# Kernel tuning notes

Hardware: AMD Instinct MI355X
Metric: run time of the kernel (lower is better)

## Reference

```python
import jax, jax.numpy as jnp
import numpy as np
import math

DIM = 384
HEADS = 12
WIN = (12, 12)
N = WIN[0] * WIN[1]  # 144
TABLE = (2 * WIN[0] - 1) * (2 * WIN[1] - 1)  # 529
B_ = 512
NW = 16
CPB_HIDDEN = 512


def setup_inputs() -> dict:
    key = jax.random.key(0)
    ks = jax.random.split(key, 12)
    x = jax.random.normal(ks[0], (B_, N, DIM), dtype=jnp.float32)
    relative_coords_table = jax.random.uniform(ks[1], (1, 2 * WIN[0] - 1, 2 * WIN[1] - 1, 2), dtype=jnp.float32) * 2.0 - 1.0
    relative_position_index = jax.random.randint(ks[2], (N, N), 0, TABLE, dtype=jnp.int64)
    mask = jnp.zeros((NW, N, N), dtype=jnp.float32)
    # learned params
    qkv_w = jax.random.normal(ks[3], (3 * DIM, DIM), dtype=jnp.float32) * (1.0 / math.sqrt(DIM))
    q_bias = jnp.zeros((DIM,), dtype=jnp.float32)
    k_bias = jnp.zeros((DIM,), dtype=jnp.float32)
    v_bias = jnp.zeros((DIM,), dtype=jnp.float32)
    logit_scale = jnp.full((HEADS, 1, 1), math.log(10.0), dtype=jnp.float32)
    cpb_w1 = jax.random.normal(ks[4], (CPB_HIDDEN, 2), dtype=jnp.float32) * 0.5
    cpb_b1 = jnp.zeros((CPB_HIDDEN,), dtype=jnp.float32)
    cpb_w2 = jax.random.normal(ks[5], (HEADS, CPB_HIDDEN), dtype=jnp.float32) * (1.0 / math.sqrt(CPB_HIDDEN))
    proj_w = jax.random.normal(ks[6], (DIM, DIM), dtype=jnp.float32) * (1.0 / math.sqrt(DIM))
    proj_b = jnp.zeros((DIM,), dtype=jnp.float32)
    return {
        'x': x,
        'relative_coords_table': relative_coords_table,
        'relative_position_index': relative_position_index,
        'mask': mask,
        'qkv_w': qkv_w, 'q_bias': q_bias, 'k_bias': k_bias, 'v_bias': v_bias,
        'logit_scale': logit_scale,
        'cpb_w1': cpb_w1, 'cpb_b1': cpb_b1, 'cpb_w2': cpb_w2,
        'proj_w': proj_w, 'proj_b': proj_b,
    }


def reference(x, relative_coords_table, relative_position_index, mask,
              qkv_w, q_bias, k_bias, v_bias, logit_scale,
              cpb_w1, cpb_b1, cpb_w2, proj_w, proj_b):
    Bw, n, C = x.shape
    H = HEADS
    d = C // H
    qkv_bias = jnp.concatenate([q_bias, k_bias, v_bias])
    qkv = x @ qkv_w.T + qkv_bias  # (Bw, n, 3C)
    qkv = qkv.reshape(Bw, n, 3, H, d).transpose(2, 0, 3, 1, 4)  # (3, Bw, H, n, d)
    q, k, v = qkv[0], qkv[1], qkv[2]
    # cosine attention
    qn = q / jnp.linalg.norm(q, axis=-1, keepdims=True)
    kn = k / jnp.linalg.norm(k, axis=-1, keepdims=True)
    attn = jnp.einsum('bhnd,bhmd->bhnm', qn, kn)
    scale = jnp.exp(jnp.minimum(logit_scale, math.log(1.0 / 0.01)))  # (H,1,1)
    attn = attn * scale[None]
    # CPB-MLP relative position bias
    h1 = jax.nn.relu(relative_coords_table @ cpb_w1.T + cpb_b1)  # (1,23,23,512)
    table = (h1 @ cpb_w2.T).reshape(-1, H)  # (529, H)
    rpb = table[relative_position_index.reshape(-1)].reshape(n, n, H)
    rpb = 16.0 * jax.nn.sigmoid(rpb.transpose(2, 0, 1))  # (H, n, n)
    attn = attn + rpb[None]
    # shifted-window mask
    nW = mask.shape[0]
    attn = attn.reshape(Bw // nW, nW, H, n, n) + mask[None, :, None]
    attn = attn.reshape(Bw, H, n, n)
    attn = jax.nn.softmax(attn, axis=-1)
    out = jnp.einsum('bhnm,bhmd->bhnd', attn, v)
    out = out.transpose(0, 2, 1, 3).reshape(Bw, n, C)
    out = out @ proj_w.T + proj_b
    return out
```

## Files before the change

### kernel.cpp

```cpp
#include <hip/hip_runtime.h>

#define DIMC 384
#define NHEADS 12
#define NTOK 144
#define TABLEN 529
#define BWIN 512
#define NWIN 16
#define CPBH 512

typedef unsigned short u16;
typedef unsigned int u32;
typedef __attribute__((ext_vector_type(8))) short short8;
typedef __attribute__((ext_vector_type(4))) float f32x4;

#define MFMA(a, b, c) __builtin_amdgcn_mfma_f32_16x16x32_bf16((a), (b), (c), 0, 0, 0)

__device__ __forceinline__ u16 f2bf(float f) {
  union { float f; u32 u; } v; v.f = f;
  u32 r = v.u + 0x7fffu + ((v.u >> 16) & 1u);
  return (u16)(r >> 16);
}
__device__ __forceinline__ u32 pk2(float a, float b) {
  return (u32)f2bf(a) | ((u32)f2bf(b) << 16);
}
__device__ __forceinline__ u32 cvtpk(float lo, float hi) {
  u32 r;
  asm("v_cvt_pk_bf16_f32 %0, %1, %2" : "=v"(r) : "v"(lo), "v"(hi));
  return r;
}

__global__ __launch_bounds__(256) void cvt_bf16(const float* __restrict__ in,
                                                u16* __restrict__ out, int n8) {
  int i = blockIdx.x * 256 + threadIdx.x;
  if (i >= n8) return;
  const float4* p = (const float4*)(in + (size_t)i * 8);
  float4 a = p[0], b = p[1];
  uint4 r;
  r.x = pk2(a.x, a.y); r.y = pk2(a.z, a.w);
  r.z = pk2(b.x, b.y); r.w = pk2(b.z, b.w);
  *(uint4*)(out + (size_t)i * 8) = r;
}

__global__ __launch_bounds__(256) void cpb_kernel(const float* __restrict__ rct,
                                                  const float* __restrict__ w1,
                                                  const float* __restrict__ b1,
                                                  const float* __restrict__ w2,
                                                  const float* __restrict__ logit_scale,
                                                  float* __restrict__ bias_tab,
                                                  float* __restrict__ scalev) {
  __shared__ float h1[CPBH];
  int i = blockIdx.x;
  int tid = threadIdx.x;
  if (i == 0 && tid < NHEADS)
    scalev[tid] = __expf(fminf(logit_scale[tid], 4.60517018598809f));
  float c0 = rct[2 * i], c1 = rct[2 * i + 1];
  for (int k = tid; k < CPBH; k += 256)
    h1[k] = fmaxf(0.f, fmaf(c0, w1[2 * k], fmaf(c1, w1[2 * k + 1], b1[k])));
  __syncthreads();
  int wv = tid >> 6, lane = tid & 63;
#pragma unroll
  for (int hh = 0; hh < 3; ++hh) {
    int h = wv * 3 + hh;
    const float* w2h = w2 + (size_t)h * CPBH;
    float acc = 0.f;
#pragma unroll
    for (int k = 0; k < CPBH; k += 64) acc = fmaf(h1[k + lane], w2h[k + lane], acc);
    acc += __shfl_xor(acc, 1); acc += __shfl_xor(acc, 2); acc += __shfl_xor(acc, 4);
    acc += __shfl_xor(acc, 8); acc += __shfl_xor(acc, 16); acc += __shfl_xor(acc, 32);
    if (lane == 0) bias_tab[i * NHEADS + h] = 16.f / (1.f + __expf(-acc));
  }
}

__global__ __launch_bounds__(256) void cbias_kernel(const int* __restrict__ rpi,
                                                    const float* __restrict__ bias_tab,
                                                    const float* __restrict__ mask,
                                                    float* __restrict__ cb) {
  int e4 = blockIdx.x * 256 + threadIdx.x;
  if (e4 >= NWIN * NHEADS * NTOK * NTOK / 4) return;
  int m0 = (e4 * 4) % NTOK;
  int t = (e4 * 4) / NTOK;
  int n = t % NTOK; t /= NTOK;
  int h = t % NHEADS;
  int w = t / NHEADS;
  int4 idx = *(const int4*)(rpi + n * NTOK + m0);
  float4 mk = *(const float4*)(mask + ((size_t)(w * NTOK + n)) * NTOK + m0);
  float4 r;
  r.x = bias_tab[idx.x * NHEADS + h] + mk.x;
  r.y = bias_tab[idx.y * NHEADS + h] + mk.y;
  r.z = bias_tab[idx.z * NHEADS + h] + mk.z;
  r.w = bias_tab[idx.w * NHEADS + h] + mk.w;
  *(float4*)(cb + (size_t)e4 * 4) = r;
}

__global__ __launch_bounds__(576) void attn_fused(
    const u16* __restrict__ xb, const u16* __restrict__ wb,
    const float* __restrict__ q_bias, const float* __restrict__ k_bias,
    const float* __restrict__ v_bias, const float* __restrict__ cb,
    const float* __restrict__ scalev, u16* __restrict__ ctx) {
  __shared__ u16 smem[22656];
  u16* qn = smem;
  u16* kn = smem + 5760;
  u16* vT = smem + 11520;
  u16* Pc = smem + 16896;
  u16* xs = smem;
  u16* wsm = smem + 9216;

  int bid = blockIdx.x;
  int xcd = bid & 7;
  int i = bid >> 3;
  int wsub = i / 192;
  int j = i - wsub * 192;
  int bI = j / 6;
  int hp = j - bI * 6;
  int w = xcd * 2 + wsub;
  int b = bI * NWIN + w;
  int h0 = hp * 2;

  int tid = threadIdx.x;
  int lane = tid & 63, wv = tid >> 6;
  int g = lane >> 4, c = lane & 15;
  int rbase = wv * 16;
  int wr3 = wv / 3, wc3 = wv % 3;

  f32x4 acc[3][4];
#pragma unroll
  for (int mi = 0; mi < 3; ++mi)
#pragma unroll
    for (int ni = 0; ni < 4; ++ni) acc[mi][ni] = (f32x4){0.f, 0.f, 0.f, 0.f};

  int r4 = tid >> 2, b4 = tid & 3;
  bool hasW1 = tid < 192;
  int wr1 = 144 + r4;
  int wg0 = (r4 >> 6) * DIMC + (h0 + ((r4 >> 5) & 1)) * 32 + (r4 & 31);
  int wg1 = (wr1 >> 6) * DIMC + (h0 + ((wr1 >> 5) & 1)) * 32 + (wr1 & 31);
  const u16* xg = xb + ((size_t)b * NTOK + r4) * DIMC + b4 * 8;
  const u16* wgp0 = wb + (size_t)wg0 * DIMC + b4 * 8;
  const u16* wgp1 = wb + (size_t)wg1 * DIMC + b4 * 8;
  int xo0 = r4 * 64 + 8 * (b4 ^ (r4 & 7));
  int xo1 = r4 * 64 + 8 * ((b4 + 4) ^ (r4 & 7));
  int w1o0 = wr1 * 64 + 8 * (b4 ^ (wr1 & 7));
  int w1o1 = wr1 * 64 + 8 * ((b4 + 4) ^ (wr1 & 7));

  uint4 pxA, pw0A, pw1A, pxB, pw0B, pw1B;
  pxA = *(const uint4*)(xg);
  pw0A = *(const uint4*)(wgp0);
  if (hasW1) pw1A = *(const uint4*)(wgp1);
  pxB = *(const uint4*)(xg + 32);
  pw0B = *(const uint4*)(wgp0 + 32);
  if (hasW1) pw1B = *(const uint4*)(wgp1 + 32);

#pragma unroll
  for (int tt = 0; tt < 6; ++tt) {
    *(uint4*)(xs + xo0) = pxA;
    *(uint4*)(wsm + xo0) = pw0A;
    if (hasW1) *(uint4*)(wsm + w1o0) = pw1A;
    __syncthreads();
    if (tt < 5) {
      int k0 = (2 * tt + 2) * 32;
      pxA = *(const uint4*)(xg + k0);
      pw0A = *(const uint4*)(wgp0 + k0);
      if (hasW1) pw1A = *(const uint4*)(wgp1 + k0);
    }
    {
      short8 ax[3];
#pragma unroll
      for (int mi = 0; mi < 3; ++mi) {
        int arow = wr3 * 48 + mi * 16 + c;
        ax[mi] = *(const short8*)(xs + arow * 64 + 8 * (g ^ (arow & 7)));
      }
#pragma unroll
      for (int ni = 0; ni < 4; ++ni) {
        int row = wc3 * 64 + ni * 16 + c;
        short8 bw = *(const short8*)(wsm + row * 64 + 8 * (g ^ (row & 7)));
#pragma unroll
        for (int mi = 0; mi < 3; ++mi) acc[mi][ni] = MFMA(ax[mi], bw, acc[mi][ni]);
      }
    }
    *(uint4*)(xs + xo1) = pxB;
    *(uint4*)(wsm + xo1) = pw0B;
    if (hasW1) *(uint4*)(wsm + w1o1) = pw1B;
    __syncthreads();
    if (tt < 5) {
      int k0 = (2 * tt + 3) * 32;
      pxB = *(const uint4*)(xg + k0);
      pw0B = *(const uint4*)(wgp0 + k0);
      if (hasW1) pw1B = *(const uint4*)(wgp1 + k0);
    }
    {
      short8 ax[3];
#pragma unroll
      for (int mi = 0; mi < 3; ++mi) {
        int arow = wr3 * 48 + mi * 16 + c;
        ax[mi] = *(const short8*)(xs + arow * 64 + 8 * ((g + 4) ^ (arow & 7)));
      }
#pragma unroll
      for (int ni = 0; ni < 4; ++ni) {
        int row = wc3 * 64 + ni * 16 + c;
        short8 bw = *(const short8*)(wsm + row * 64 + 8 * ((g + 4) ^ (row & 7)));
#pragma unroll
        for (int mi = 0; mi < 3; ++mi) acc[mi][ni] = MFMA(ax[mi], bw, acc[mi][ni]);
      }
    }
  }
  __syncthreads();

#pragma unroll
  for (int hh = 0; hh < 2; ++hh) {
    int h = h0 + hh;
    if (hh) __syncthreads();

    float sch = scalev[h];
    if (wc3 == 0) {
      float qb0 = q_bias[h * 32 + c], qb1 = q_bias[h * 32 + 16 + c];
#pragma unroll
      for (int mi = 0; mi < 3; ++mi) {
#pragma unroll
        for (int r = 0; r < 4; ++r) {
          int row = wr3 * 48 + mi * 16 + g * 4 + r;
          float q0 = acc[mi][hh * 2][r] + qb0, q1 = acc[mi][hh * 2 + 1][r] + qb1;
          float ssq = q0 * q0 + q1 * q1;
          ssq += __shfl_xor(ssq, 1); ssq += __shfl_xor(ssq, 2);
          ssq += __shfl_xor(ssq, 4); ssq += __shfl_xor(ssq, 8);
          float siq = sch / sqrtf(ssq);
          qn[row * 40 + c] = f2bf(q0 * siq);
          qn[row * 40 + 16 + c] = f2bf(q1 * siq);
        }
      }
    } else if (wc3 == 1) {
      float kb0 = k_bias[h * 32 + c], kb1 = k_bias[h * 32 + 16 + c];
#pragma unroll
      for (int mi = 0; mi < 3; ++mi) {
#pragma unroll
        for (int r = 0; r < 4; ++r) {
          int row = wr3 * 48 + mi * 16 + g * 4 + r;
          float k0v = acc[mi][hh * 2][r] + kb0, k1v = acc[mi][hh * 2 + 1][r] + kb1;
          float ssk = k0v * k0v + k1v * k1v;
          ssk += __shfl_xor(ssk, 1); ssk += __shfl_xor(ssk, 2);
          ssk += __shfl_xor(ssk, 4); ssk += __shfl_xor(ssk, 8);
          float sik = 1.f / sqrtf(ssk);
          kn[row * 40 + c] = f2bf(k0v * sik);
          kn[row * 40 + 16 + c] = f2bf(k1v * sik);
        }
      }
    } else {
      float vb0 = v_bias[h * 32 + c], vb1 = v_bias[h * 32 + 16 + c];
#pragma unroll
      for (int mi = 0; mi < 3; ++mi) {
        float v0a[4], v1a[4];
#pragma unroll
        for (int r = 0; r < 4; ++r) {
          v0a[r] = acc[mi][hh * 2][r] + vb0;
          v1a[r] = acc[mi][hh * 2 + 1][r] + vb1;
        }
        int m0 = wr3 * 48 + mi * 16 + g * 4;
        u16* p0 = vT + c * 168 + m0;
        u16* p1 = vT + (16 + c) * 168 + m0;
        *(u32*)p0 = cvtpk(v0a[0], v0a[1]);
        *(u32*)(p0 + 2) = cvtpk(v0a[2], v0a[3]);
        *(u32*)p1 = cvtpk(v1a[0], v1a[1]);
        *(u32*)(p1 + 2) = cvtpk(v1a[2], v1a[3]);
      }
    }
    if (hh == 0 && tid < 32) {
      uint4 z4 = {0u, 0u, 0u, 0u};
      *(uint4*)(vT + tid * 168 + 144) = z4;
      *(uint4*)(vT + tid * 168 + 152) = z4;
      *(uint4*)(vT + tid * 168 + 160) = z4;
    }
    __syncthreads();

    short8 aq = *(const short8*)(qn + (rbase + c) * 40 + g * 8);
    f32x4 S[9];
#pragma unroll
    for (int mt = 0; mt < 9; ++mt) {
      short8 bk = *(const short8*)(kn + (mt * 16 + c) * 40 + g * 8);
      f32x4 z = (f32x4){0.f, 0.f, 0.f, 0.f};
      S[mt] = MFMA(aq, bk, z);
    }

    const float* cbh = cb + (((size_t)w * NHEADS + h) * NTOK) * NTOK;
#pragma unroll
    for (int r = 0; r < 4; ++r) {
      int row = rbase + g * 4 + r;
      const float* crow = cbh + (size_t)row * NTOK + c;
      float sv[9];
      float mx = -1e30f;
#pragma unroll
      for (int mt = 0; mt < 9; ++mt) {
        float s = S[mt][r] + crow[mt * 16];
        sv[mt] = s;
        mx = fmaxf(mx, s);
      }
      mx = fmaxf(mx, __shfl_xor(mx, 1)); mx = fmaxf(mx, __shfl_xor(mx, 2));
      mx = fmaxf(mx, __shfl_xor(mx, 4)); mx = fmaxf(mx, __shfl_xor(mx, 8));
      float sum = 0.f;
#pragma unroll
      for (int mt = 0; mt < 9; ++mt) {
        float p = __expf(sv[mt] - mx);
        sv[mt] = p;
        sum += p;
      }
      sum += __shfl_xor(sum, 1); sum += __shfl_xor(sum, 2);
      sum += __shfl_xor(sum, 4); sum += __shfl_xor(sum, 8);
      float rinv = 1.f / sum;
#pragma unroll
      for (int mt = 0; mt < 9; ++mt) S[mt][r] = sv[mt] * rinv;
    }

    f32x4 po[2];
    po[0] = (f32x4){0.f, 0.f, 0.f, 0.f};
    po[1] = (f32x4){0.f, 0.f, 0.f, 0.f};
    for (int ck = 0; ck < 5; ++ck) {
#pragma unroll
      for (int mt2 = 0; mt2 < 2; ++mt2) {
        int MT = ck * 2 + mt2;
#pragma unroll
        for (int r = 0; r < 4; ++r) {
          int row = rbase + g * 4 + r;
          float p = (MT < 9) ? S[MT][r] : 0.f;
          Pc[row * 40 + mt2 * 16 + c] = f2bf(p);
        }
      }
      short8 pa = *(const short8*)(Pc + (rbase + c) * 40 + g * 8);
#pragma unroll
      for (int dt = 0; dt < 2; ++dt) {
        short8 vb = *(const short8*)(vT + (dt * 16 + c) * 168 + ck * 32 + g * 8);
        po[dt] = MFMA(pa, vb, po[dt]);
      }
    }

#pragma unroll
    for (int dt = 0; dt < 2; ++dt)
#pragma unroll
      for (int r = 0; r < 4; ++r) {
        int n = rbase + g * 4 + r;
        ctx[((size_t)b * NTOK + n) * DIMC + h * 32 + dt * 16 + c] = f2bf(po[dt][r]);
      }
  }
}

__global__ __launch_bounds__(256) void proj_gemm(const u16* __restrict__ ctx,
                                                 const u16* __restrict__ pwb,
                                                 const float* __restrict__ proj_b,
                                                 float* __restrict__ out) {
  __shared__ u16 As[128 * 64];
  __shared__ u16 Bs[128 * 64];
  int bid = blockIdx.x;
  int xcd8 = bid & 7;
  int ii = bid >> 3;
  int nblk = ii % 3;
  int mblk = xcd8 + 8 * (ii / 3);
  size_t gm0 = (size_t)mblk * 128;
  int gn0 = nblk * 128;
  int tid = threadIdx.x, lane = tid & 63, wid = tid >> 6;
  int wr = wid >> 1, wc = wid & 1, g = lane >> 4, c = lane & 15;
  f32x4 acc[4][4];
#pragma unroll
  for (int i = 0; i < 4; ++i)
#pragma unroll
    for (int j = 0; j < 4; ++j) acc[i][j] = (f32x4){0.f, 0.f, 0.f, 0.f};

  for (int t = 0; t < 6; ++t) {
    int k0 = t * 64;
#pragma unroll
    for (int p = 0; p < 4; ++p) {
      int row = p * 32 + (tid >> 3);
      int seg = (tid & 7) * 8;
      uint4 va = *(const uint4*)(ctx + (gm0 + row) * DIMC + k0 + seg);
      *(uint4*)(As + row * 64 + seg) = va;
      uint4 vb = *(const uint4*)(pwb + (size_t)(gn0 + row) * DIMC + k0 + seg);
      *(uint4*)(Bs + row * 64 + seg) = vb;
    }
    __syncthreads();
#pragma unroll
    for (int kk = 0; kk < 64; kk += 32) {
      short8 a[4], bfr[4];
#pragma unroll
      for (int mi = 0; mi < 4; ++mi)
        a[mi] = *(const short8*)(As + (wr * 64 + mi * 16 + c) * 64 + kk + g * 8);
#pragma unroll
      for (int ni = 0; ni < 4; ++ni)
        bfr[ni] = *(const short8*)(Bs + (wc * 64 + ni * 16 + c) * 64 + kk + g * 8);
#pragma unroll
      for (int mi = 0; mi < 4; ++mi)
#pragma unroll
        for (int ni = 0; ni < 4; ++ni)
          acc[mi][ni] = MFMA(a[mi], bfr[ni], acc[mi][ni]);
    }
    __syncthreads();
  }
#pragma unroll
  for (int mi = 0; mi < 4; ++mi)
#pragma unroll
    for (int ni = 0; ni < 4; ++ni) {
      int gcol = gn0 + wc * 64 + ni * 16 + c;
      float bv = proj_b[gcol];
#pragma unroll
      for (int r = 0; r < 4; ++r) {
        size_t grow = gm0 + wr * 64 + mi * 16 + g * 4 + r;
        out[grow * DIMC + gcol] = acc[mi][ni][r] + bv;
      }
    }
}

extern "C" void kernel_launch(void* const* d_in, const int* in_sizes, int n_in,
                              void* d_out, int out_size, void* d_ws, size_t ws_size,
                              hipStream_t stream) {
  const float* x = (const float*)d_in[0];
  const float* rct = (const float*)d_in[1];
  const int* rpi = (const int*)d_in[2];
  const float* mask = (const float*)d_in[3];
  const float* qkv_w = (const float*)d_in[4];
  const float* q_bias = (const float*)d_in[5];
  const float* k_bias = (const float*)d_in[6];
  const float* v_bias = (const float*)d_in[7];
  const float* logit_scale = (const float*)d_in[8];
  const float* cpb_w1 = (const float*)d_in[9];
  const float* cpb_b1 = (const float*)d_in[10];
  const float* cpb_w2 = (const float*)d_in[11];
  const float* proj_w = (const float*)d_in[12];
  const float* proj_b = (const float*)d_in[13];
  float* out = (float*)d_out;

  char* ws = (char*)d_ws;
  size_t off = 0;
  auto alloc = [&](size_t bytes) {
    void* p = ws + off;
    off = (off + bytes + 255) & ~(size_t)255;
    return p;
  };
  const size_t NX = (size_t)BWIN * NTOK * DIMC;
  u16* xb = (u16*)alloc(NX * 2);
  u16* wqb = (u16*)alloc((size_t)3 * DIMC * DIMC * 2);
  u16* pwb = (u16*)alloc((size_t)DIMC * DIMC * 2);
  u16* ctx = (u16*)alloc(NX * 2);
  float* cbv = (float*)alloc((size_t)NWIN * NHEADS * NTOK * NTOK * 4);
  float* bias_tab = (float*)alloc((size_t)TABLEN * NHEADS * 4);
  float* scalev = (float*)alloc(64 * 4);

  cvt_bf16<<<(int)(NX / 8 + 255) / 256, 256, 0, stream>>>(x, xb, (int)(NX / 8));
  cvt_bf16<<<(3 * DIMC * DIMC / 8 + 255) / 256, 256, 0, stream>>>(qkv_w, wqb, 3 * DIMC * DIMC / 8);
  cvt_bf16<<<(DIMC * DIMC / 8 + 255) / 256, 256, 0, stream>>>(proj_w, pwb, DIMC * DIMC / 8);
  cpb_kernel<<<TABLEN, 256, 0, stream>>>(
      rct, cpb_w1, cpb_b1, cpb_w2, logit_scale, bias_tab, scalev);
  cbias_kernel<<<(NWIN * NHEADS * NTOK * NTOK / 4 + 255) / 256, 256, 0, stream>>>(
      rpi, bias_tab, mask, cbv);
  attn_fused<<<BWIN * 6, 576, 0, stream>>>(
      xb, wqb, q_bias, k_bias, v_bias, cbv, scalev, ctx);
  proj_gemm<<<(BWIN * NTOK / 128) * 3, 256, 0, stream>>>(ctx, pwb, proj_b, out);
}
```

Baseline: 309.1 us.

## Process both heads' attention together with double-buffered Q/K/V in LDS

Stores normalized Q, K and transposed V for both heads of a block into separate LDS buffers, so one barrier replaces the per-head barrier. The QK^T MFMAs and the softmax for the two heads are interleaved, which gives more independent work for latency hiding. In exchange, LDS use grows from about 45KB to about 79KB per block and register pressure rises from holding two score arrays, which may lower occupancy.

```diff
diff --git a/kernel.cpp b/kernel.cpp
--- a/kernel.cpp
+++ b/kernel.cpp
@@ -97,11 +97,14 @@
     const float* __restrict__ q_bias, const float* __restrict__ k_bias,
     const float* __restrict__ v_bias, const float* __restrict__ cb,
     const float* __restrict__ scalev, u16* __restrict__ ctx) {
-  __shared__ u16 smem[22656];
-  u16* qn = smem;
-  u16* kn = smem + 5760;
-  u16* vT = smem + 11520;
-  u16* Pc = smem + 16896;
+  __shared__ u16 smem[39552];
+  u16* qnA = smem;
+  u16* knA = smem + 5760;
+  u16* vTA = smem + 11520;
+  u16* qnB = smem + 16896;
+  u16* knB = smem + 22656;
+  u16* vTB = smem + 28416;
+  u16* Pc = smem + 33792;
   u16* xs = smem;
   u16* wsm = smem + 9216;
 
@@ -204,13 +207,12 @@
   }
   __syncthreads();
 
-#pragma unroll
-  for (int hh = 0; hh < 2; ++hh) {
-    int h = h0 + hh;
-    if (hh) __syncthreads();
-
-    float sch = scalev[h];
-    if (wc3 == 0) {
+  if (wc3 == 0) {
+#pragma unroll
+    for (int hh = 0; hh < 2; ++hh) {
+      int h = h0 + hh;
+      u16* qn = hh ? qnB : qnA;
+      float sch = scalev[h];
       float qb0 = q_bias[h * 32 + c], qb1 = q_bias[h * 32 + 16 + c];
 #pragma unroll
       for (int mi = 0; mi < 3; ++mi) {
@@ -226,7 +228,12 @@
           qn[row * 40 + 16 + c] = f2bf(q1 * siq);
         }
       }
-    } else if (wc3 == 1) {
+    }
+  } else if (wc3 == 1) {
+#pragma unroll
+    for (int hh = 0; hh < 2; ++hh) {
+      int h = h0 + hh;
+      u16* kn = hh ? knB : knA;
       float kb0 = k_bias[h * 32 + c], kb1 = k_bias[h * 32 + 16 + c];
 #pragma unroll
       for (int mi = 0; mi < 3; ++mi) {
@@ -242,7 +249,12 @@
           kn[row * 40 + 16 + c] = f2bf(k1v * sik);
         }
       }
-    } else {
+    }
+  } else {
+#pragma unroll
+    for (int hh = 0; hh < 2; ++hh) {
+      int h = h0 + hh;
+      u16* vT = hh ? vTB : vTA;
       float vb0 = v_bias[h * 32 + c], vb1 = v_bias[h * 32 + 16 + c];
 #pragma unroll
       for (int mi = 0; mi < 3; ++mi) {
@@ -261,52 +273,79 @@
         *(u32*)(p1 + 2) = cvtpk(v1a[2], v1a[3]);
       }
     }
-    if (hh == 0 && tid < 32) {
-      uint4 z4 = {0u, 0u, 0u, 0u};
-      *(uint4*)(vT + tid * 168 + 144) = z4;
-      *(uint4*)(vT + tid * 168 + 152) = z4;
-      *(uint4*)(vT + tid * 168 + 160) = z4;
-    }
-    __syncthreads();
-
-    short8 aq = *(const short8*)(qn + (rbase + c) * 40 + g * 8);
-    f32x4 S[9];
+  }
+  if (tid < 32) {
+    uint4 z4 = {0u, 0u, 0u, 0u};
+    *(uint4*)(vTA + tid * 168 + 144) = z4;
+    *(uint4*)(vTA + tid * 168 + 152) = z4;
+    *(uint4*)(vTA + tid * 168 + 160) = z4;
+  } else if (tid < 64) {
+    int d = tid - 32;
+    uint4 z4 = {0u, 0u, 0u, 0u};
+    *(uint4*)(vTB + d * 168 + 144) = z4;
+    *(uint4*)(vTB + d * 168 + 152) = z4;
+    *(uint4*)(vTB + d * 168 + 160) = z4;
+  }
+  __syncthreads();
+
+  short8 aqA = *(const short8*)(qnA + (rbase + c) * 40 + g * 8);
+  short8 aqB = *(const short8*)(qnB + (rbase + c) * 40 + g * 8);
+  f32x4 S_A[9], S_B[9];
+#pragma unroll
+  for (int mt = 0; mt < 9; ++mt) {
+    short8 bkA = *(const short8*)(knA + (mt * 16 + c) * 40 + g * 8);
+    f32x4 z = (f32x4){0.f, 0.f, 0.f, 0.f};
+    S_A[mt] = MFMA(aqA, bkA, z);
+    short8 bkB = *(const short8*)(knB + (mt * 16 + c) * 40 + g * 8);
+    f32x4 z2 = (f32x4){0.f, 0.f, 0.f, 0.f};
+    S_B[mt] = MFMA(aqB, bkB, z2);
+  }
+
+  const float* cbhA = cb + (((size_t)w * NHEADS + h0) * NTOK) * NTOK;
+  const float* cbhB = cb + (((size_t)w * NHEADS + h0 + 1) * NTOK) * NTOK;
+#pragma unroll
+  for (int r = 0; r < 4; ++r) {
+    int row = rbase + g * 4 + r;
+    const float* crowA = cbhA + (size_t)row * NTOK + c;
+    const float* crowB = cbhB + (size_t)row * NTOK + c;
+    float svA[9], svB[9];
+    float mxA = -1e30f, mxB = -1e30f;
 #pragma unroll
     for (int mt = 0; mt < 9; ++mt) {
-      short8 bk = *(const short8*)(kn + (mt * 16 + c) * 40 + g * 8);
-      f32x4 z = (f32x4){0.f, 0.f, 0.f, 0.f};
-      S[mt] = MFMA(aq, bk, z);
-    }
-
-    const float* cbh = cb + (((size_t)w * NHEADS + h) * NTOK) * NTOK;
-#pragma unroll
-    for (int r = 0; r < 4; ++r) {
-      int row = rbase + g * 4 + r;
-      const float* crow = cbh + (size_t)row * NTOK + c;
-      float sv[9];
-      float mx = -1e30f;
-#pragma unroll
-      for (int mt = 0; mt < 9; ++mt) {
-        float s = S[mt][r] + crow[mt * 16];
-        sv[mt] = s;
-        mx = fmaxf(mx, s);
-      }
-      mx = fmaxf(mx, __shfl_xor(mx, 1)); mx = fmaxf(mx, __shfl_xor(mx, 2));
-      mx = fmaxf(mx, __shfl_xor(mx, 4)); mx = fmaxf(mx, __shfl_xor(mx, 8));
-      float sum = 0.f;
-#pragma unroll
-      for (int mt = 0; mt < 9; ++mt) {
-        float p = __expf(sv[mt] - mx);
-        sv[mt] = p;
-        sum += p;
-      }
-      sum += __shfl_xor(sum, 1); sum += __shfl_xor(sum, 2);
-      sum += __shfl_xor(sum, 4); sum += __shfl_xor(sum, 8);
-      float rinv = 1.f / sum;
-#pragma unroll
-      for (int mt = 0; mt < 9; ++mt) S[mt][r] = sv[mt] * rinv;
-    }
-
+      float sA = S_A[mt][r] + crowA[mt * 16];
+      svA[mt] = sA;
+      mxA = fmaxf(mxA, sA);
+      float sB = S_B[mt][r] + crowB[mt * 16];
+      svB[mt] = sB;
+      mxB = fmaxf(mxB, sB);
+    }
+    mxA = fmaxf(mxA, __shfl_xor(mxA, 1)); mxA = fmaxf(mxA, __shfl_xor(mxA, 2));
+    mxA = fmaxf(mxA, __shfl_xor(mxA, 4)); mxA = fmaxf(mxA, __shfl_xor(mxA, 8));
+    mxB = fmaxf(mxB, __shfl_xor(mxB, 1)); mxB = fmaxf(mxB, __shfl_xor(mxB, 2));
+    mxB = fmaxf(mxB, __shfl_xor(mxB, 4)); mxB = fmaxf(mxB, __shfl_xor(mxB, 8));
+    float sumA = 0.f, sumB = 0.f;
+#pragma unroll
+    for (int mt = 0; mt < 9; ++mt) {
+      float pA = __expf(svA[mt] - mxA);
+      svA[mt] = pA;
+      sumA += pA;
+      float pB = __expf(svB[mt] - mxB);
+      svB[mt] = pB;
+      sumB += pB;
+    }
+    sumA += __shfl_xor(sumA, 1); sumA += __shfl_xor(sumA, 2);
+    sumA += __shfl_xor(sumA, 4); sumA += __shfl_xor(sumA, 8);
+    sumB += __shfl_xor(sumB, 1); sumB += __shfl_xor(sumB, 2);
+    sumB += __shfl_xor(sumB, 4); sumB += __shfl_xor(sumB, 8);
+    float rinvA = 1.f / sumA, rinvB = 1.f / sumB;
+#pragma unroll
+    for (int mt = 0; mt < 9; ++mt) {
+      S_A[mt][r] = svA[mt] * rinvA;
+      S_B[mt][r] = svB[mt] * rinvB;
+    }
+  }
+
+  {
     f32x4 po[2];
     po[0] = (f32x4){0.f, 0.f, 0.f, 0.f};
     po[1] = (f32x4){0.f, 0.f, 0.f, 0.f};
@@ -317,24 +356,53 @@
 #pragma unroll
         for (int r = 0; r < 4; ++r) {
           int row = rbase + g * 4 + r;
-          float p = (MT < 9) ? S[MT][r] : 0.f;
+          float p = (MT < 9) ? S_A[MT][r] : 0.f;
           Pc[row * 40 + mt2 * 16 + c] = f2bf(p);
         }
       }
       short8 pa = *(const short8*)(Pc + (rbase + c) * 40 + g * 8);
 #pragma unroll
       for (int dt = 0; dt < 2; ++dt) {
-        short8 vb = *(const short8*)(vT + (dt * 16 + c) * 168 + ck * 32 + g * 8);
+        short8 vb = *(const short8*)(vTA + (dt * 16 + c) * 168 + ck * 32 + g * 8);
         po[dt] = MFMA(pa, vb, po[dt]);
       }
     }
-
 #pragma unroll
     for (int dt = 0; dt < 2; ++dt)
 #pragma unroll
       for (int r = 0; r < 4; ++r) {
         int n = rbase + g * 4 + r;
-        ctx[((size_t)b * NTOK + n) * DIMC + h * 32 + dt * 16 + c] = f2bf(po[dt][r]);
+        ctx[((size_t)b * NTOK + n) * DIMC + h0 * 32 + dt * 16 + c] = f2bf(po[dt][r]);
+      }
+  }
+  {
+    f32x4 po[2];
+    po[0] = (f32x4){0.f, 0.f, 0.f, 0.f};
+    po[1] = (f32x4){0.f, 0.f, 0.f, 0.f};
+    for (int ck = 0; ck < 5; ++ck) {
+#pragma unroll
+      for (int mt2 = 0; mt2 < 2; ++mt2) {
+        int MT = ck * 2 + mt2;
+#pragma unroll
+        for (int r = 0; r < 4; ++r) {
+          int row = rbase + g * 4 + r;
+          float p = (MT < 9) ? S_B[MT][r] : 0.f;
+          Pc[row * 40 + mt2 * 16 + c] = f2bf(p);
+        }
+      }
+      short8 pa = *(const short8*)(Pc + (rbase + c) * 40 + g * 8);
+#pragma unroll
+      for (int dt = 0; dt < 2; ++dt) {
+        short8 vb = *(const short8*)(vTB + (dt * 16 + c) * 168 + ck * 32 + g * 8);
+        po[dt] = MFMA(pa, vb, po[dt]);
+      }
+    }
+#pragma unroll
+    for (int dt = 0; dt < 2; ++dt)
+#pragma unroll
+      for (int r = 0; r < 4; ++r) {
+        int n = rbase + g * 4 + r;
+        ctx[((size_t)b * NTOK + n) * DIMC + (h0 + 1) * 32 + dt * 16 + c] = f2bf(po[dt][r]);
       }
   }
 }
```

After: 317.4 us. +2.7%, slower.
